# Kernel optimization log

Hardware: AMD Instinct MI355X
Metric: run time of the kernel (lower is better)

Reference implementation:

```python
import jax, jax.numpy as jnp
import numpy as np

NEG_SLOPE = 0.01  # torch nn.LeakyReLU default


def setup_inputs() -> dict:
    key = jax.random.key(0)
    k1, k2, k3, k4 = jax.random.split(key, 4)
    N, D = 8192, 64
    x = jax.random.normal(k1, (N, D), dtype=jnp.float32)
    W = jax.random.normal(k2, (D, D), dtype=jnp.float32) * (1.0 / np.sqrt(D))
    b = jax.random.normal(k3, (D,), dtype=jnp.float32) * 0.01
    a = jax.random.normal(k4, (2 * D, 1), dtype=jnp.float32)
    return {"x": x, "W": W, "b": b, "a": a}


def reference(x, W, b, a):
    # h = Linear(x): torch stores weight as [out, in], y = x @ W.T + b
    h = x @ W.T + b  # [N, D]
    D = h.shape[1]
    a1 = a[:D, 0]   # weights on the column node (e_x[i,j] = x_j)
    a2 = a[D:, 0]   # weights on the row node    (e_y[i,j] = x_i)
    s1 = h @ a1     # [N], contribution of node j
    s2 = h @ a2     # [N], contribution of node i
    # score[i, j] = a1.h_j + a2.h_i  (equivalent to expand+concat+matmul)
    scores = s2[:, None] + s1[None, :]                       # [N, N]
    scores = jnp.where(scores >= 0, scores, NEG_SLOPE * scores)  # leaky_relu
    att = jax.nn.softmax(scores, axis=1)                     # softmax over j
    # NOTE: forward multiplies attention with the ORIGINAL x, not h
    return att @ x                                           # [N, D]
```

## Files before the change

### kernel.cpp

```cpp
#include <hip/hip_runtime.h>

#define NEG_SLOPE 0.01f

constexpr int N = 8192;
constexpr int D = 64;

typedef __bf16 bf16x8 __attribute__((ext_vector_type(8)));
typedef float f32x4 __attribute__((ext_vector_type(4)));

__global__ __launch_bounds__(256) void gat_prep(
    const float* __restrict__ x, const float* __restrict__ W_,
    const float* __restrict__ b, const float* __restrict__ a,
    float* __restrict__ s1, float* __restrict__ s2,
    unsigned int* __restrict__ maxkey) {
  __shared__ float w1s[D], w2s[D], cs[2];
  const int t = threadIdx.x;
  if (t < 128) {
    const int sel = t >> 6, d = t & 63;
    const float* av = a + sel * D;
    float acc = 0.f;
#pragma unroll
    for (int k = 0; k < D; ++k) acc += W_[k * D + d] * av[k];
    (sel ? w2s : w1s)[d] = acc;
  }
  if (t == 128 || t == 129) {
    const int sel = t - 128;
    float acc = 0.f;
    for (int d = 0; d < D; ++d) acc += b[d] * a[sel * D + d];
    cs[sel] = acc;
  }
  __syncthreads();

  const int i = blockIdx.x * 256 + t;
  const float4* xr = (const float4*)(x + (size_t)i * D);
  float v1 = cs[0], v2 = cs[1];
#pragma unroll
  for (int k = 0; k < 16; ++k) {
    float4 v = xr[k];
    v1 += v.x * w1s[4 * k + 0] + v.y * w1s[4 * k + 1] + v.z * w1s[4 * k + 2] + v.w * w1s[4 * k + 3];
    v2 += v.x * w2s[4 * k + 0] + v.y * w2s[4 * k + 1] + v.z * w2s[4 * k + 2] + v.w * w2s[4 * k + 3];
  }
  s1[i] = v1;
  s2[i] = v2;

  float m = v1;
#pragma unroll
  for (int off = 32; off; off >>= 1) m = fmaxf(m, __shfl_xor(m, off, 64));
  if ((t & 63) == 0) {
    unsigned int bb = __float_as_uint(m);
    unsigned int key = (bb & 0x80000000u) ? ~bb : (bb | 0x80000000u);
    atomicMax(maxkey, key);
  }
}

__global__ __launch_bounds__(256) void gat_pack(
    const float* __restrict__ x, bf16x8* __restrict__ xf) {
  const int gid = blockIdx.x * 256 + threadIdx.x;
  const int lane = gid & 63;
  const int dt = (gid >> 6) & 3;
  const int wi = gid >> 8;
  const int jb = wi * 32 + ((lane >> 4) << 3);
  const int col = dt * 16 + (lane & 15);
  bf16x8 f;
#pragma unroll
  for (int q = 0; q < 8; ++q) f[q] = (__bf16)x[(size_t)(jb + q) * D + col];
  xf[gid] = f;
}

__global__ __launch_bounds__(256, 2) void gat_main(
    const bf16x8* __restrict__ xf, const float* __restrict__ s1g,
    const float* __restrict__ s2g, const unsigned int* __restrict__ maxkey,
    float* __restrict__ out) {
  __shared__ float accT[4][16][64];
  __shared__ float zt[4][16];

  const int t = threadIdx.x;
  const int lane = t & 63;
  const int w = t >> 6;
  const int arow = lane & 15;
  const int grp = lane >> 4;
  const int ibase = blockIdx.x * 16;

  const unsigned int key = *maxkey;
  const unsigned int mb = (key & 0x80000000u) ? (key ^ 0x80000000u) : ~key;
  const float maxs1 = __uint_as_float(mb);

  const float s2v = s2g[ibase + arow];
  const float tmax = s2v + maxs1;
  const float mneg = -fmaxf(tmax, NEG_SLOPE * tmax);

  f32x4 acc0 = {0.f, 0.f, 0.f, 0.f};
  f32x4 acc1 = {0.f, 0.f, 0.f, 0.f};
  f32x4 acc2 = {0.f, 0.f, 0.f, 0.f};
  f32x4 acc3 = {0.f, 0.f, 0.f, 0.f};
  float zz = 0.f;

#pragma unroll 2
  for (int c = w; c < N / 32; c += 4) {
    const int fb = c << 8;
    bf16x8 xb0 = xf[fb + 0 * 64 + lane];
    bf16x8 xb1 = xf[fb + 1 * 64 + lane];
    bf16x8 xb2 = xf[fb + 2 * 64 + lane];
    bf16x8 xb3 = xf[fb + 3 * 64 + lane];

    const float* s1p = s1g + c * 32 + grp * 8;
    const float4 sa = *(const float4*)s1p;
    const float4 sb = *(const float4*)(s1p + 4);

    float pv[8];
    {
      const float* sv = &sa.x;
#pragma unroll
      for (int q = 0; q < 4; ++q) {
        const float tt = s2v + sv[q];
        pv[q] = __expf(fmaxf(tt, NEG_SLOPE * tt) + mneg);
      }
      const float* sw = &sb.x;
#pragma unroll
      for (int q = 0; q < 4; ++q) {
        const float tt = s2v + sw[q];
        pv[4 + q] = __expf(fmaxf(tt, NEG_SLOPE * tt) + mneg);
      }
    }
    bf16x8 pa;
#pragma unroll
    for (int q = 0; q < 8; ++q) {
      pa[q] = (__bf16)pv[q];
      zz += pv[q];
    }

    acc0 = __builtin_amdgcn_mfma_f32_16x16x32_bf16(pa, xb0, acc0, 0, 0, 0);
    acc1 = __builtin_amdgcn_mfma_f32_16x16x32_bf16(pa, xb1, acc1, 0, 0, 0);
    acc2 = __builtin_amdgcn_mfma_f32_16x16x32_bf16(pa, xb2, acc2, 0, 0, 0);
    acc3 = __builtin_amdgcn_mfma_f32_16x16x32_bf16(pa, xb3, acc3, 0, 0, 0);
  }

  zz += __shfl_xor(zz, 16, 64);
  zz += __shfl_xor(zz, 32, 64);
  if (lane < 16) zt[w][lane] = zz;

#pragma unroll
  for (int reg = 0; reg < 4; ++reg) {
    accT[w][grp * 4 + reg][0 * 16 + arow] = acc0[reg];
    accT[w][grp * 4 + reg][1 * 16 + arow] = acc1[reg];
    accT[w][grp * 4 + reg][2 * 16 + arow] = acc2[reg];
    accT[w][grp * 4 + reg][3 * 16 + arow] = acc3[reg];
  }
  __syncthreads();

#pragma unroll
  for (int k = 0; k < 4; ++k) {
    const int r = w * 4 + k;
    const float s = accT[0][r][lane] + accT[1][r][lane] + accT[2][r][lane] + accT[3][r][lane];
    const float z = zt[0][r] + zt[1][r] + zt[2][r] + zt[3][r];
    out[(size_t)(ibase + r) * D + lane] = s / z;
  }
}

extern "C" void kernel_launch(void* const* d_in, const int* in_sizes, int n_in,
                              void* d_out, int out_size, void* d_ws, size_t ws_size,
                              hipStream_t stream) {
  const float* x = (const float*)d_in[0];
  const float* W = (const float*)d_in[1];
  const float* b = (const float*)d_in[2];
  const float* a = (const float*)d_in[3];

  unsigned int* maxkey = (unsigned int*)d_ws;
  float* s1 = (float*)d_ws + 16;
  float* s2 = s1 + N;
  bf16x8* xf = (bf16x8*)((char*)d_ws + (1u << 20));
  float* out = (float*)d_out;

  hipMemsetAsync(d_ws, 0, 16, stream);
  gat_prep<<<N / 256, 256, 0, stream>>>(x, W, b, a, s1, s2, maxkey);
  gat_pack<<<(N / 32) * 4 * 64 / 256, 256, 0, stream>>>(x, xf);
  gat_main<<<N / 16, 256, 0, stream>>>(xf, s1, s2, maxkey, out);
}
```

Measured before the change: 96.23 us.

## Fuse prep, pack and main into one cooperative kernel with grid sync

Merges the three kernels and the memset into a single cooperative launch. Each block computes s1/s2 for its 16 rows, packs its share of x into bf16 MFMA layout, and writes a per-block max of s1. A grid-wide sync then lets every block reduce the 512 block maxima and run the attention MFMA loop. This removes launch gaps, the memset and the atomicMax. In exchange it adds the cost of a grid barrier and needs all 512 blocks to be co-resident.

Measured after the change: 174.4 us. +81.3%, slower.

```diff
diff --git a/kernel.cpp b/kernel.cpp
--- a/kernel.cpp
+++ b/kernel.cpp
@@ -1,20 +1,34 @@
 #include <hip/hip_runtime.h>
+#include <hip/hip_cooperative_groups.h>
+
+namespace cg = cooperative_groups;
 
 #define NEG_SLOPE 0.01f
 
 constexpr int N = 8192;
 constexpr int D = 64;
+constexpr int RB = 16;
+constexpr int NB = N / RB;
 
 typedef __bf16 bf16x8 __attribute__((ext_vector_type(8)));
 typedef float f32x4 __attribute__((ext_vector_type(4)));
 
-__global__ __launch_bounds__(256) void gat_prep(
+__global__ __launch_bounds__(256, 2) void gat_fused(
     const float* __restrict__ x, const float* __restrict__ W_,
     const float* __restrict__ b, const float* __restrict__ a,
-    float* __restrict__ s1, float* __restrict__ s2,
-    unsigned int* __restrict__ maxkey) {
+    float* __restrict__ s1g, float* __restrict__ blockmax,
+    bf16x8* __restrict__ xf, float* __restrict__ out) {
   __shared__ float w1s[D], w2s[D], cs[2];
+  __shared__ float s1loc[RB], s2loc[RB];
+  __shared__ float wred[4];
+  __shared__ float accT[4][RB][64];
+  __shared__ float zt[4][RB];
+
   const int t = threadIdx.x;
+  const int bid = blockIdx.x;
+  const int lane = t & 63;
+  const int w = t >> 6;
+
   if (t < 128) {
     const int sel = t >> 6, d = t & 63;
     const float* av = a + sel * D;
@@ -31,62 +45,63 @@
   }
   __syncthreads();
 
-  const int i = blockIdx.x * 256 + t;
-  const float4* xr = (const float4*)(x + (size_t)i * D);
-  float v1 = cs[0], v2 = cs[1];
+  {
+    const int r = t >> 4, seg = t & 15;
+    const int gi = bid * RB + r;
+    const float4 xv = *(const float4*)(x + (size_t)gi * D + seg * 4);
+    float p1 = xv.x * w1s[seg * 4 + 0] + xv.y * w1s[seg * 4 + 1] +
+               xv.z * w1s[seg * 4 + 2] + xv.w * w1s[seg * 4 + 3];
+    float p2 = xv.x * w2s[seg * 4 + 0] + xv.y * w2s[seg * 4 + 1] +
+               xv.z * w2s[seg * 4 + 2] + xv.w * w2s[seg * 4 + 3];
 #pragma unroll
-  for (int k = 0; k < 16; ++k) {
-    float4 v = xr[k];
-    v1 += v.x * w1s[4 * k + 0] + v.y * w1s[4 * k + 1] + v.z * w1s[4 * k + 2] + v.w * w1s[4 * k + 3];
-    v2 += v.x * w2s[4 * k + 0] + v.y * w2s[4 * k + 1] + v.z * w2s[4 * k + 2] + v.w * w2s[4 * k + 3];
+    for (int off = 8; off; off >>= 1) {
+      p1 += __shfl_xor(p1, off, 64);
+      p2 += __shfl_xor(p2, off, 64);
+    }
+    if (seg == 0) {
+      const float v1 = p1 + cs[0], v2 = p2 + cs[1];
+      s1g[gi] = v1;
+      s1loc[r] = v1;
+      s2loc[r] = v2;
+    }
   }
-  s1[i] = v1;
-  s2[i] = v2;
 
-  float m = v1;
+  if (t < 128) {
+    const int h = bid & 1, w0 = bid >> 1;
+    const int dt = t >> 5, ll = t & 31;
+    const int fl = h * 32 + ll;
+    const int jb = w0 * 32 + ((fl >> 4) << 3);
+    const int col = dt * 16 + (fl & 15);
+    bf16x8 f;
 #pragma unroll
-  for (int off = 32; off; off >>= 1) m = fmaxf(m, __shfl_xor(m, off, 64));
-  if ((t & 63) == 0) {
-    unsigned int bb = __float_as_uint(m);
-    unsigned int key = (bb & 0x80000000u) ? ~bb : (bb | 0x80000000u);
-    atomicMax(maxkey, key);
+    for (int q = 0; q < 8; ++q) f[q] = (__bf16)x[(size_t)(jb + q) * D + col];
+    xf[(w0 << 8) | (dt << 6) | fl] = f;
   }
-}
+  __syncthreads();
+  if (t == 0) {
+    float m = s1loc[0];
+#pragma unroll
+    for (int r = 1; r < RB; ++r) m = fmaxf(m, s1loc[r]);
+    blockmax[bid] = m;
+  }
 
-__global__ __launch_bounds__(256) void gat_pack(
-    const float* __restrict__ x, bf16x8* __restrict__ xf) {
-  const int gid = blockIdx.x * 256 + threadIdx.x;
-  const int lane = gid & 63;
-  const int dt = (gid >> 6) & 3;
-  const int wi = gid >> 8;
-  const int jb = wi * 32 + ((lane >> 4) << 3);
-  const int col = dt * 16 + (lane & 15);
-  bf16x8 f;
+  __threadfence();
+  cg::this_grid().sync();
+
+  float gm;
+  {
+    float v = fmaxf(blockmax[t], blockmax[t + 256]);
 #pragma unroll
-  for (int q = 0; q < 8; ++q) f[q] = (__bf16)x[(size_t)(jb + q) * D + col];
-  xf[gid] = f;
-}
+    for (int off = 32; off; off >>= 1) v = fmaxf(v, __shfl_xor(v, off, 64));
+    if (lane == 0) wred[w] = v;
+    __syncthreads();
+    gm = fmaxf(fmaxf(wred[0], wred[1]), fmaxf(wred[2], wred[3]));
+  }
 
-__global__ __launch_bounds__(256, 2) void gat_main(
-    const bf16x8* __restrict__ xf, const float* __restrict__ s1g,
-    const float* __restrict__ s2g, const unsigned int* __restrict__ maxkey,
-    float* __restrict__ out) {
-  __shared__ float accT[4][16][64];
-  __shared__ float zt[4][16];
-
-  const int t = threadIdx.x;
-  const int lane = t & 63;
-  const int w = t >> 6;
   const int arow = lane & 15;
   const int grp = lane >> 4;
-  const int ibase = blockIdx.x * 16;
-
-  const unsigned int key = *maxkey;
-  const unsigned int mb = (key & 0x80000000u) ? (key ^ 0x80000000u) : ~key;
-  const float maxs1 = __uint_as_float(mb);
-
-  const float s2v = s2g[ibase + arow];
-  const float tmax = s2v + maxs1;
+  const float s2v = s2loc[arow];
+  const float tmax = s2v + gm;
   const float mneg = -fmaxf(tmax, NEG_SLOPE * tmax);
 
   f32x4 acc0 = {0.f, 0.f, 0.f, 0.f};
@@ -153,7 +168,7 @@
     const int r = w * 4 + k;
     const float s = accT[0][r][lane] + accT[1][r][lane] + accT[2][r][lane] + accT[3][r][lane];
     const float z = zt[0][r] + zt[1][r] + zt[2][r] + zt[3][r];
-    out[(size_t)(ibase + r) * D + lane] = s / z;
+    out[(size_t)(bid * RB + r) * D + lane] = s / z;
   }
 }
 
@@ -165,14 +180,12 @@
   const float* b = (const float*)d_in[2];
   const float* a = (const float*)d_in[3];
 
-  unsigned int* maxkey = (unsigned int*)d_ws;
-  float* s1 = (float*)d_ws + 16;
-  float* s2 = s1 + N;
+  float* s1 = (float*)d_ws;
+  float* blockmax = s1 + N;
   bf16x8* xf = (bf16x8*)((char*)d_ws + (1u << 20));
   float* out = (float*)d_out;
 
-  hipMemsetAsync(d_ws, 0, 16, stream);
-  gat_prep<<<N / 256, 256, 0, stream>>>(x, W, b, a, s1, s2, maxkey);
-  gat_pack<<<(N / 32) * 4 * 64 / 256, 256, 0, stream>>>(x, xf);
-  gat_main<<<N / 16, 256, 0, stream>>>(xf, s1, s2, maxkey, out);
+  void* args[] = {(void*)&x, (void*)&W, (void*)&b, (void*)&a,
+                  (void*)&s1, (void*)&blockmax, (void*)&xf, (void*)&out};
+  hipLaunchCooperativeKernel((void*)gat_fused, dim3(NB), dim3(256), args, 0, stream);
 }
```
